# Kernel tuning notes

Measured on AMD Instinct MI355X. Metric: run time of the kernel, lower is better.

## Reference

```python
import jax, jax.numpy as jnp
import numpy as np


def setup_inputs() -> dict:
    key = jax.random.key(0)
    kq, kk, kv = jax.random.split(key, 3)
    B, L, Q, H, E = 8, 128, 8, 8, 64
    S, P = 128, 8
    queries = jax.random.normal(kq, (B, L, Q, H, E), dtype=jnp.float32)
    keys = jax.random.normal(kk, (B, S, P, H, E), dtype=jnp.float32)
    values = jax.random.normal(kv, (B, S, P, H, E), dtype=jnp.float32)
    attn_mask = jnp.zeros((1,), dtype=bool)  # unused by the module
    return {"queries": queries, "keys": keys, "values": values, "attn_mask": attn_mask}


def reference(queries, keys, values, attn_mask):
    # queries: [B,L,Q,H,E]; keys/values: [B,S,P,H,E]
    B, L, Q, H, E = queries.shape
    S, P = values.shape[1], values.shape[2]
    scale = 1.0 / np.sqrt(E).astype(np.float32)
    # scores: [B,S,P,L,Q,H]
    scores = jnp.einsum('blqhe,bsphe->bsplqh', queries, keys)
    # softmax over joint (S,P) axis
    scaled = (scale * scores).reshape(B, S * P, L, Q, H)
    attn = jax.nn.softmax(scaled, axis=1).reshape(B, S, P, L, Q, H)
    # dropout is identity in eval / with p=0.0
    V = jnp.einsum('bsphe,bsplqh->blqhe', values, attn)
    return V
```

## Files before the change

kernel.cpp:

```cpp
#include <hip/hip_runtime.h>
#include <hip/hip_bf16.h>

typedef __attribute__((ext_vector_type(4))) float f32x4;
typedef __attribute__((ext_vector_type(16))) float f32x16;
typedef __attribute__((ext_vector_type(8))) short bf16x8;
typedef __attribute__((ext_vector_type(4))) unsigned u32x4;

#define MFMA32(a, b, c) __builtin_amdgcn_mfma_f32_32x32x16_bf16(a, b, c, 0, 0, 0)
#define EXP2(x) __builtin_amdgcn_exp2f(x)

constexpr int NQ = 1024;
constexpr int NK = 1024;
constexpr int RS = 512;
constexpr int Ec = 64;
constexpr int KT = 64;
constexpr int NR = 8;
constexpr float QSCALE2 = 0.125f * 1.4426950408889634f;
constexpr float DEFER_THR = 8.0f;

__device__ __forceinline__ short f2bf(float x) {
    return (short)__builtin_bit_cast(unsigned short, __float2bfloat16(x));
}

__device__ __forceinline__ bf16x8 pack2(float4 a, float4 b) {
    bf16x8 r;
    r[0] = f2bf(a.x); r[1] = f2bf(a.y); r[2] = f2bf(a.z); r[3] = f2bf(a.w);
    r[4] = f2bf(b.x); r[5] = f2bf(b.y); r[6] = f2bf(b.z); r[7] = f2bf(b.w);
    return r;
}

__device__ __forceinline__ bf16x8 pack2s(float4 a, float4 b, float s) {
    bf16x8 r;
    r[0] = f2bf(a.x * s); r[1] = f2bf(a.y * s); r[2] = f2bf(a.z * s); r[3] = f2bf(a.w * s);
    r[4] = f2bf(b.x * s); r[5] = f2bf(b.y * s); r[6] = f2bf(b.z * s); r[7] = f2bf(b.w * s);
    return r;
}

__device__ __forceinline__ unsigned cvtpk(float a, float b) {
    unsigned lo = (unsigned short)__builtin_bit_cast(unsigned short, __float2bfloat16(a));
    unsigned hi = (unsigned short)__builtin_bit_cast(unsigned short, __float2bfloat16(b));
    return lo | (hi << 16);
}

__device__ __forceinline__ void gload16(const short* src, short* dst) {
    __builtin_amdgcn_global_load_lds((const __attribute__((address_space(1))) void*)src,
                                     (__attribute__((address_space(3))) void*)dst, 16, 0, 0);
}

__global__ __launch_bounds__(256, 4)
void cvt_kv(const float* __restrict__ Kg, const float* __restrict__ Vg,
            short* __restrict__ Kbf, short* __restrict__ Vt) {
    __shared__ __attribute__((aligned(16))) short Vl[64][72];
    const int tid  = threadIdx.x;
    const int head = blockIdx.x >> 4;
    const int kb   = blockIdx.x & 15;
    const int b    = head >> 3, h = head & 7;
    const int row  = tid >> 2, q = tid & 3;

    const size_t gin = (((size_t)(b * NK + kb * 64 + row)) * 8 + h) * 64 + q * 16;
    const float4* kp = (const float4*)(Kg + gin);
    float4 k0 = kp[0], k1 = kp[1], k2 = kp[2], k3 = kp[3];
    short* kout = Kbf + ((size_t)head * NK + kb * 64 + row) * 64 + q * 16;
    ((bf16x8*)kout)[0] = pack2(k0, k1);
    ((bf16x8*)kout)[1] = pack2(k2, k3);

    const float4* vp = (const float4*)(Vg + gin);
    float4 v0 = vp[0], v1 = vp[1], v2 = vp[2], v3 = vp[3];
    const float vv[16] = {v0.x, v0.y, v0.z, v0.w, v1.x, v1.y, v1.z, v1.w,
                          v2.x, v2.y, v2.z, v2.w, v3.x, v3.y, v3.z, v3.w};
#pragma unroll
    for (int j = 0; j < 16; ++j) Vl[q * 16 + j][row] = f2bf(vv[j]);
    __syncthreads();
    short* vout = Vt + ((size_t)head * Ec + row) * NK + kb * 64 + q * 16;
    ((bf16x8*)vout)[0] = *(const bf16x8*)&Vl[row][q * 16];
    ((bf16x8*)vout)[1] = *(const bf16x8*)&Vl[row][q * 16 + 8];
}

__global__ __launch_bounds__(512, 4)
void fully_attn_kernel(const float* __restrict__ Qg, const short* __restrict__ Kbf,
                       const short* __restrict__ Vt, float* __restrict__ Og) {
    __shared__ __attribute__((aligned(16))) short Kl[2][2][64][64];
    __shared__ __attribute__((aligned(16))) short Vl[2][2][64][64];

    const int tid  = threadIdx.x;
    const int lane = tid & 63;
    const int wv   = tid >> 6;
    const int grp  = wv & 3;
    const int par  = wv >> 2;
    const int ql   = lane & 31;
    const int hi   = lane >> 5;
    const int swz  = (lane & 7) << 4;

    const int bid  = blockIdx.x;
    const int head = (bid & 7) * 8 + (bid >> 6);
    const int qb   = (bid >> 3) & 7;
    const int b    = head >> 3, h = head & 7;

    const size_t headQ = (size_t)b * NQ * RS + (size_t)h * Ec;
    const short* KbfH = Kbf + (size_t)head * NK * Ec;
    const short* VtH  = Vt + (size_t)head * Ec * NK;

    const int qrow = qb * 128 + grp * 32 + ql;
    const float* qp = Qg + headQ + (size_t)qrow * RS;
    bf16x8 qf[4];
#pragma unroll
    for (int j = 0; j < 4; ++j) {
        const float4* q4 = (const float4*)(qp + j * 16 + hi * 8);
        qf[j] = pack2s(q4[0], q4[1], QSCALE2);
    }

    const int srow = wv * 8 + (lane >> 3);
    const int sj   = (lane & 7) ^ ((lane >> 3) & 7);

#define STAGE(buf, rr)                                                           \
    {                                                                            \
        gload16(KbfH + (size_t)((2 * (rr)) * KT + srow) * 64 + sj * 8,           \
                &Kl[buf][0][wv * 8][0]);                                         \
        gload16(KbfH + (size_t)((2 * (rr) + 1) * KT + srow) * 64 + sj * 8,       \
                &Kl[buf][1][wv * 8][0]);                                         \
        gload16(VtH + (size_t)srow * NK + (2 * (rr)) * KT + sj * 8,              \
                &Vl[buf][0][wv * 8][0]);                                         \
        gload16(VtH + (size_t)srow * NK + (2 * (rr) + 1) * KT + sj * 8,          \
                &Vl[buf][1][wv * 8][0]);                                         \
    }

    STAGE(0, 0);
    __syncthreads();

    float m_r = -1e30f, l_r = 0.0f;
    f32x16 o0 = (f32x16)(0.0f), o1 = (f32x16)(0.0f);

    int cur = 0;
    for (int r = 0; r < NR; ++r) {
        if (r + 1 < NR) STAGE(cur ^ 1, r + 1);

        bf16x8 kf[2][4];
#pragma unroll
        for (int kt = 0; kt < 2; ++kt) {
            const char* kr = (const char*)&Kl[cur][par][kt * 32 + ql][0];
#pragma unroll
            for (int j = 0; j < 4; ++j)
                kf[kt][j] = *(const bf16x8*)(kr + ((j * 32 + hi * 16) ^ swz));
        }
        f32x16 p[2];
        __builtin_amdgcn_s_setprio(1);
#pragma unroll
        for (int kt = 0; kt < 2; ++kt) {
            f32x16 acc = (f32x16)(0.0f);
#pragma unroll
            for (int j = 0; j < 4; ++j) acc = MFMA32(kf[kt][j], qf[j], acc);
            p[kt] = acc;
        }
        __builtin_amdgcn_s_setprio(0);

        bf16x8 vf0[4], vf1[4];
#pragma unroll
        for (int m = 0; m < 4; ++m) {
            const int cb = (m * 32 + hi * 16) ^ swz;
            vf0[m] = *(const bf16x8*)((const char*)&Vl[cur][par][ql][0] + cb);
            vf1[m] = *(const bf16x8*)((const char*)&Vl[cur][par][32 + ql][0] + cb);
        }

        float pm0 = p[0][0], pm1 = p[0][1], pm2 = p[0][2], pm3 = p[0][3];
#pragma unroll
        for (int kt = 0; kt < 2; ++kt)
#pragma unroll
            for (int i = (kt == 0 ? 4 : 0); i < 16; i += 4) {
                pm0 = fmaxf(pm0, p[kt][i + 0]);
                pm1 = fmaxf(pm1, p[kt][i + 1]);
                pm2 = fmaxf(pm2, p[kt][i + 2]);
                pm3 = fmaxf(pm3, p[kt][i + 3]);
            }
        float pm = fmaxf(fmaxf(pm0, pm1), fmaxf(pm2, pm3));
        pm = fmaxf(pm, __shfl_xor(pm, 32));

        if (!__all(pm <= m_r + DEFER_THR)) {
            const float mn = fmaxf(m_r, pm);
            const float alpha = EXP2(m_r - mn);
            l_r *= alpha;
#pragma unroll
            for (int i = 0; i < 16; ++i) { o0[i] *= alpha; o1[i] *= alpha; }
            m_r = mn;
        }

        float rs0 = 0.f, rs1 = 0.f, rs2 = 0.f, rs3 = 0.f;
#pragma unroll
        for (int kt = 0; kt < 2; ++kt)
#pragma unroll
            for (int i = 0; i < 16; i += 4) {
                float e0 = EXP2(p[kt][i + 0] - m_r);
                float e1 = EXP2(p[kt][i + 1] - m_r);
                float e2 = EXP2(p[kt][i + 2] - m_r);
                float e3 = EXP2(p[kt][i + 3] - m_r);
                p[kt][i + 0] = e0; p[kt][i + 1] = e1;
                p[kt][i + 2] = e2; p[kt][i + 3] = e3;
                rs0 += e0; rs1 += e1; rs2 += e2; rs3 += e3;
            }
        l_r += (rs0 + rs1) + (rs2 + rs3);

        __builtin_amdgcn_s_setprio(1);
#pragma unroll
        for (int m = 0; m < 4; ++m) {
            const int kt = m >> 1, r0 = (m & 1) * 8;
            unsigned a0 = cvtpk(p[kt][r0 + 0], p[kt][r0 + 1]);
            unsigned a1 = cvtpk(p[kt][r0 + 2], p[kt][r0 + 3]);
            unsigned b0 = cvtpk(p[kt][r0 + 4], p[kt][r0 + 5]);
            unsigned b1 = cvtpk(p[kt][r0 + 6], p[kt][r0 + 7]);
            asm("v_permlane32_swap_b32 %0, %1" : "+v"(a0), "+v"(b0));
            asm("v_permlane32_swap_b32 %0, %1" : "+v"(a1), "+v"(b1));
            u32x4 w = {a0, a1, b0, b1};
            bf16x8 pf = __builtin_bit_cast(bf16x8, w);
            o0 = MFMA32(vf0[m], pf, o0);
            o1 = MFMA32(vf1[m], pf, o1);
        }
        __builtin_amdgcn_s_setprio(0);

        __syncthreads();
        cur ^= 1;
    }

    l_r += __shfl_xor(l_r, 32);

    float* scrO  = (float*)&Kl[0][0][0][0];
    float* scrML = (float*)&Vl[0][0][0][0];
    const int slot = grp * 64 + lane;
    if (par == 1) {
#pragma unroll
        for (int i = 0; i < 16; ++i) {
            scrO[i * 256 + slot]         = o0[i];
            scrO[(16 + i) * 256 + slot]  = o1[i];
        }
        scrML[slot * 2 + 0] = m_r;
        scrML[slot * 2 + 1] = l_r;
    }
    __syncthreads();
    if (par == 0) {
        const float m_b = scrML[slot * 2 + 0];
        const float l_b = scrML[slot * 2 + 1];
        const float M  = fmaxf(m_r, m_b);
        const float aa = EXP2(m_r - M);
        const float ab = EXP2(m_b - M);
        const float inv = 1.0f / (aa * l_r + ab * l_b);

        float* op = Og + headQ + (size_t)qrow * RS;
#pragma unroll
        for (int bnk = 0; bnk < 4; ++bnk) {
            float4 s0, s1;
#pragma unroll
            for (int j = 0; j < 4; ++j) {
                const int i = bnk * 4 + j;
                ((float*)&s0)[j] = (aa * o0[i] + ab * scrO[i * 256 + slot]) * inv;
                ((float*)&s1)[j] = (aa * o1[i] + ab * scrO[(16 + i) * 256 + slot]) * inv;
            }
            *(float4*)(op + bnk * 8 + hi * 4)      = s0;
            *(float4*)(op + 32 + bnk * 8 + hi * 4) = s1;
        }
    }
}

extern "C" void kernel_launch(void* const* d_in, const int* in_sizes, int n_in,
                              void* d_out, int out_size, void* d_ws, size_t ws_size,
                              hipStream_t stream) {
    const float* Qg = (const float*)d_in[0];
    const float* Kg = (const float*)d_in[1];
    const float* Vg = (const float*)d_in[2];
    float* Og = (float*)d_out;

    short* Kbf = (short*)d_ws;
    short* Vt  = (short*)d_ws + (size_t)64 * NK * Ec;

    hipLaunchKernelGGL(cvt_kv, dim3(64 * 16), dim3(256), 0, stream, Kg, Vg, Kbf, Vt);
    hipLaunchKernelGGL(fully_attn_kernel, dim3(512), dim3(512), 0, stream,
                       Qg, Kbf, Vt, Og);
}
```

Baseline: 51.73 us.

## Halve attention block to 64 queries and 4 waves, doubling grid size

Restructures the attention kernel from 512-thread blocks covering 128 queries, each key-parity wave pair processing 128 keys per stage, to 256-thread blocks covering 64 queries with 64 keys per stage and 16 rounds. The grid grows to 1024 blocks and per-block LDS halves, which raises the number of blocks available to fill CUs and may allow more resident blocks. In exchange, each K/V tile is loaded by twice as many blocks, so global traffic rises, and there are more barriers per key processed.

```diff
diff --git a/kernel.cpp b/kernel.cpp
--- a/kernel.cpp
+++ b/kernel.cpp
@@ -14,7 +14,7 @@
 constexpr int RS = 512;
 constexpr int Ec = 64;
 constexpr int KT = 64;
-constexpr int NR = 8;
+constexpr int NR = NK / KT;
 constexpr float QSCALE2 = 0.125f * 1.4426950408889634f;
 constexpr float DEFER_THR = 8.0f;
 
@@ -76,31 +76,31 @@
     ((bf16x8*)vout)[1] = *(const bf16x8*)&Vl[row][q * 16 + 8];
 }
 
-__global__ __launch_bounds__(512, 4)
+__global__ __launch_bounds__(256, 4)
 void fully_attn_kernel(const float* __restrict__ Qg, const short* __restrict__ Kbf,
                        const short* __restrict__ Vt, float* __restrict__ Og) {
-    __shared__ __attribute__((aligned(16))) short Kl[2][2][64][64];
-    __shared__ __attribute__((aligned(16))) short Vl[2][2][64][64];
+    __shared__ __attribute__((aligned(16))) short Kl[2][64][64];
+    __shared__ __attribute__((aligned(16))) short Vl[2][64][64];
 
     const int tid  = threadIdx.x;
     const int lane = tid & 63;
     const int wv   = tid >> 6;
-    const int grp  = wv & 3;
-    const int par  = wv >> 2;
+    const int grp  = wv & 1;
+    const int par  = wv >> 1;
     const int ql   = lane & 31;
     const int hi   = lane >> 5;
     const int swz  = (lane & 7) << 4;
 
     const int bid  = blockIdx.x;
-    const int head = (bid & 7) * 8 + (bid >> 6);
-    const int qb   = (bid >> 3) & 7;
+    const int head = (bid & 7) * 8 + (bid >> 7);
+    const int qb   = (bid >> 3) & 15;
     const int b    = head >> 3, h = head & 7;
 
     const size_t headQ = (size_t)b * NQ * RS + (size_t)h * Ec;
     const short* KbfH = Kbf + (size_t)head * NK * Ec;
     const short* VtH  = Vt + (size_t)head * Ec * NK;
 
-    const int qrow = qb * 128 + grp * 32 + ql;
+    const int qrow = qb * 64 + grp * 32 + ql;
     const float* qp = Qg + headQ + (size_t)qrow * RS;
     bf16x8 qf[4];
 #pragma unroll
@@ -109,19 +109,19 @@
         qf[j] = pack2s(q4[0], q4[1], QSCALE2);
     }
 
-    const int srow = wv * 8 + (lane >> 3);
+    const int srow = wv * 16 + (lane >> 3);
     const int sj   = (lane & 7) ^ ((lane >> 3) & 7);
 
 #define STAGE(buf, rr)                                                           \
     {                                                                            \
-        gload16(KbfH + (size_t)((2 * (rr)) * KT + srow) * 64 + sj * 8,           \
-                &Kl[buf][0][wv * 8][0]);                                         \
-        gload16(KbfH + (size_t)((2 * (rr) + 1) * KT + srow) * 64 + sj * 8,       \
-                &Kl[buf][1][wv * 8][0]);                                         \
-        gload16(VtH + (size_t)srow * NK + (2 * (rr)) * KT + sj * 8,              \
-                &Vl[buf][0][wv * 8][0]);                                         \
-        gload16(VtH + (size_t)srow * NK + (2 * (rr) + 1) * KT + sj * 8,          \
-                &Vl[buf][1][wv * 8][0]);                                         \
+        gload16(KbfH + (size_t)((rr) * KT + srow) * 64 + sj * 8,                 \
+                &Kl[buf][wv * 16][0]);                                           \
+        gload16(KbfH + (size_t)((rr) * KT + srow + 8) * 64 + sj * 8,             \
+                &Kl[buf][wv * 16 + 8][0]);                                       \
+        gload16(VtH + (size_t)srow * NK + (rr) * KT + sj * 8,                    \
+                &Vl[buf][wv * 16][0]);                                           \
+        gload16(VtH + (size_t)(srow + 8) * NK + (rr) * KT + sj * 8,              \
+                &Vl[buf][wv * 16 + 8][0]);                                       \
     }
 
     STAGE(0, 0);
@@ -134,43 +134,34 @@
     for (int r = 0; r < NR; ++r) {
         if (r + 1 < NR) STAGE(cur ^ 1, r + 1);
 
-        bf16x8 kf[2][4];
-#pragma unroll
-        for (int kt = 0; kt < 2; ++kt) {
-            const char* kr = (const char*)&Kl[cur][par][kt * 32 + ql][0];
-#pragma unroll
-            for (int j = 0; j < 4; ++j)
-                kf[kt][j] = *(const bf16x8*)(kr + ((j * 32 + hi * 16) ^ swz));
-        }
-        f32x16 p[2];
+        const char* kr = (const char*)&Kl[cur][par * 32 + ql][0];
+        bf16x8 kf0 = *(const bf16x8*)(kr + ((0 * 32 + hi * 16) ^ swz));
+        bf16x8 kf1 = *(const bf16x8*)(kr + ((1 * 32 + hi * 16) ^ swz));
+        bf16x8 kf2 = *(const bf16x8*)(kr + ((2 * 32 + hi * 16) ^ swz));
+        bf16x8 kf3 = *(const bf16x8*)(kr + ((3 * 32 + hi * 16) ^ swz));
+        f32x16 p;
         __builtin_amdgcn_s_setprio(1);
-#pragma unroll
-        for (int kt = 0; kt < 2; ++kt) {
-            f32x16 acc = (f32x16)(0.0f);
-#pragma unroll
-            for (int j = 0; j < 4; ++j) acc = MFMA32(kf[kt][j], qf[j], acc);
-            p[kt] = acc;
-        }
+        p = MFMA32(kf0, qf[0], (f32x16)(0.0f));
+        p = MFMA32(kf1, qf[1], p);
+        p = MFMA32(kf2, qf[2], p);
+        p = MFMA32(kf3, qf[3], p);
         __builtin_amdgcn_s_setprio(0);
 
-        bf16x8 vf0[4], vf1[4];
-#pragma unroll
-        for (int m = 0; m < 4; ++m) {
-            const int cb = (m * 32 + hi * 16) ^ swz;
-            vf0[m] = *(const bf16x8*)((const char*)&Vl[cur][par][ql][0] + cb);
-            vf1[m] = *(const bf16x8*)((const char*)&Vl[cur][par][32 + ql][0] + cb);
-        }
-
-        float pm0 = p[0][0], pm1 = p[0][1], pm2 = p[0][2], pm3 = p[0][3];
-#pragma unroll
-        for (int kt = 0; kt < 2; ++kt)
-#pragma unroll
-            for (int i = (kt == 0 ? 4 : 0); i < 16; i += 4) {
-                pm0 = fmaxf(pm0, p[kt][i + 0]);
-                pm1 = fmaxf(pm1, p[kt][i + 1]);
-                pm2 = fmaxf(pm2, p[kt][i + 2]);
-                pm3 = fmaxf(pm3, p[kt][i + 3]);
-            }
+        const char* vr0 = (const char*)&Vl[cur][ql][0];
+        const char* vr1 = (const char*)&Vl[cur][32 + ql][0];
+        bf16x8 vf00 = *(const bf16x8*)(vr0 + ((par * 64 + 0 * 32 + hi * 16) ^ swz));
+        bf16x8 vf01 = *(const bf16x8*)(vr0 + ((par * 64 + 1 * 32 + hi * 16) ^ swz));
+        bf16x8 vf10 = *(const bf16x8*)(vr1 + ((par * 64 + 0 * 32 + hi * 16) ^ swz));
+        bf16x8 vf11 = *(const bf16x8*)(vr1 + ((par * 64 + 1 * 32 + hi * 16) ^ swz));
+
+        float pm0 = p[0], pm1 = p[1], pm2 = p[2], pm3 = p[3];
+#pragma unroll
+        for (int i = 4; i < 16; i += 4) {
+            pm0 = fmaxf(pm0, p[i + 0]);
+            pm1 = fmaxf(pm1, p[i + 1]);
+            pm2 = fmaxf(pm2, p[i + 2]);
+            pm3 = fmaxf(pm3, p[i + 3]);
+        }
         float pm = fmaxf(fmaxf(pm0, pm1), fmaxf(pm2, pm3));
         pm = fmaxf(pm, __shfl_xor(pm, 32));
 
@@ -185,33 +176,30 @@
 
         float rs0 = 0.f, rs1 = 0.f, rs2 = 0.f, rs3 = 0.f;
 #pragma unroll
-        for (int kt = 0; kt < 2; ++kt)
-#pragma unroll
-            for (int i = 0; i < 16; i += 4) {
-                float e0 = EXP2(p[kt][i + 0] - m_r);
-                float e1 = EXP2(p[kt][i + 1] - m_r);
-                float e2 = EXP2(p[kt][i + 2] - m_r);
-                float e3 = EXP2(p[kt][i + 3] - m_r);
-                p[kt][i + 0] = e0; p[kt][i + 1] = e1;
-                p[kt][i + 2] = e2; p[kt][i + 3] = e3;
-                rs0 += e0; rs1 += e1; rs2 += e2; rs3 += e3;
-            }
+        for (int i = 0; i < 16; i += 4) {
+            float e0 = EXP2(p[i + 0] - m_r);
+            float e1 = EXP2(p[i + 1] - m_r);
+            float e2 = EXP2(p[i + 2] - m_r);
+            float e3 = EXP2(p[i + 3] - m_r);
+            p[i + 0] = e0; p[i + 1] = e1; p[i + 2] = e2; p[i + 3] = e3;
+            rs0 += e0; rs1 += e1; rs2 += e2; rs3 += e3;
+        }
         l_r += (rs0 + rs1) + (rs2 + rs3);
 
         __builtin_amdgcn_s_setprio(1);
 #pragma unroll
-        for (int m = 0; m < 4; ++m) {
-            const int kt = m >> 1, r0 = (m & 1) * 8;
-            unsigned a0 = cvtpk(p[kt][r0 + 0], p[kt][r0 + 1]);
-            unsigned a1 = cvtpk(p[kt][r0 + 2], p[kt][r0 + 3]);
-            unsigned b0 = cvtpk(p[kt][r0 + 4], p[kt][r0 + 5]);
-            unsigned b1 = cvtpk(p[kt][r0 + 6], p[kt][r0 + 7]);
+        for (int m = 0; m < 2; ++m) {
+            const int r0 = m * 8;
+            unsigned a0 = cvtpk(p[r0 + 0], p[r0 + 1]);
+            unsigned a1 = cvtpk(p[r0 + 2], p[r0 + 3]);
+            unsigned b0 = cvtpk(p[r0 + 4], p[r0 + 5]);
+            unsigned b1 = cvtpk(p[r0 + 6], p[r0 + 7]);
             asm("v_permlane32_swap_b32 %0, %1" : "+v"(a0), "+v"(b0));
             asm("v_permlane32_swap_b32 %0, %1" : "+v"(a1), "+v"(b1));
             u32x4 w = {a0, a1, b0, b1};
             bf16x8 pf = __builtin_bit_cast(bf16x8, w);
-            o0 = MFMA32(vf0[m], pf, o0);
-            o1 = MFMA32(vf1[m], pf, o1);
+            o0 = MFMA32(m ? vf01 : vf00, pf, o0);
+            o1 = MFMA32(m ? vf11 : vf10, pf, o1);
         }
         __builtin_amdgcn_s_setprio(0);
 
@@ -221,14 +209,14 @@
 
     l_r += __shfl_xor(l_r, 32);
 
-    float* scrO  = (float*)&Kl[0][0][0][0];
-    float* scrML = (float*)&Vl[0][0][0][0];
+    float* scrO  = (float*)&Kl[0][0][0];
+    float* scrML = (float*)&Vl[0][0][0];
     const int slot = grp * 64 + lane;
     if (par == 1) {
 #pragma unroll
         for (int i = 0; i < 16; ++i) {
-            scrO[i * 256 + slot]         = o0[i];
-            scrO[(16 + i) * 256 + slot]  = o1[i];
+            scrO[(grp * 32 + i) * 64 + lane]      = o0[i];
+            scrO[(grp * 32 + 16 + i) * 64 + lane] = o1[i];
         }
         scrML[slot * 2 + 0] = m_r;
         scrML[slot * 2 + 1] = l_r;
@@ -249,8 +237,10 @@
 #pragma unroll
             for (int j = 0; j < 4; ++j) {
                 const int i = bnk * 4 + j;
-                ((float*)&s0)[j] = (aa * o0[i] + ab * scrO[i * 256 + slot]) * inv;
-                ((float*)&s1)[j] = (aa * o1[i] + ab * scrO[(16 + i) * 256 + slot]) * inv;
+                ((float*)&s0)[j] =
+                    (aa * o0[i] + ab * scrO[(grp * 32 + i) * 64 + lane]) * inv;
+                ((float*)&s1)[j] =
+                    (aa * o1[i] + ab * scrO[(grp * 32 + 16 + i) * 64 + lane]) * inv;
             }
             *(float4*)(op + bnk * 8 + hi * 4)      = s0;
             *(float4*)(op + 32 + bnk * 8 + hi * 4) = s1;
@@ -270,6 +260,6 @@
     short* Vt  = (short*)d_ws + (size_t)64 * NK * Ec;
 
     hipLaunchKernelGGL(cvt_kv, dim3(64 * 16), dim3(256), 0, stream, Kg, Vg, Kbf, Vt);
-    hipLaunchKernelGGL(fully_attn_kernel, dim3(512), dim3(512), 0, stream,
+    hipLaunchKernelGGL(fully_attn_kernel, dim3(1024), dim3(256), 0, stream,
                        Qg, Kbf, Vt, Og);
 }
```

New measurement: 49.09 us. 5.1% less time.
